# Performance work log

Measured on AMD Instinct MI355X. Metric: run time of the kernel, lower is better.

The kernel has to match this reference:

```python
import jax, jax.numpy as jnp
import numpy as np

N_WIRES = 4
BATCH, SEQ, EMBED, FFN = 8, 512, 512, 2048


def setup_inputs() -> dict:
    key = jax.random.key(0)
    k_x, k_w1, k_w2 = jax.random.split(key, 3)
    x = jax.random.normal(k_x, (BATCH, SEQ, EMBED), dtype=jnp.float32)
    # Linear params (torch Linear: y = x @ W^T + b; we store pre-transposed)
    W1 = jax.random.normal(k_w1, (EMBED, FFN), dtype=jnp.float32) / np.sqrt(EMBED)
    b1 = jnp.zeros((FFN,), dtype=jnp.float32)
    W2 = jax.random.normal(k_w2, (FFN, EMBED), dtype=jnp.float32) / np.sqrt(FFN)
    b2 = jnp.zeros((EMBED,), dtype=jnp.float32)
    return {"x": x, "W1": W1, "b1": b1, "W2": W2, "b2": b2}


def reference(x, W1, b1, W2, b2):
    b, s, d = x.shape
    flat = x.reshape(b * s, d)                      # [n, d], n = b*s
    # Quantum kernel: circuit RY(x_i) then RY(-y_i) per wire on |0..0>;
    # |0..0> amplitude = prod_i cos((x_i - y_i)/2); only first n_wires feats used
    # (reset_states(1) + states.view(-1)[0] selects batch row 0 of the reshape).
    f = flat[:, :N_WIRES]                           # [n, nw]
    half_diff = (f[:, None, :] - f[None, :, :]) * 0.5   # [n, n, nw]
    gram = jnp.abs(jnp.prod(jnp.cos(half_diff), axis=-1))  # [n, n]
    out = gram @ flat                               # [n, d]
    h = jax.nn.relu(out @ W1 + b1)                  # [n, ffn]  (dropout = eval identity)
    y = h @ W2 + b2                                 # [n, d]
    return y.reshape(b, s, d)
```

## Files before the change

### kernel.cpp

```cpp
#include <hip/hip_runtime.h>
#include <hip/hip_bf16.h>
#include <stdint.h>

using bf = __bf16;
typedef __attribute__((ext_vector_type(8))) __bf16 bf16x8;
typedef __attribute__((ext_vector_type(4))) __bf16 bf16x4;
typedef __attribute__((ext_vector_type(4))) float f32x4;
typedef __attribute__((ext_vector_type(4))) int i32x4;

#define M_TOT 4096
#define D_EMB 512
#define F_FFN 2048

__device__ __forceinline__ void gload_lds16(const void* g, void* l) {
  __builtin_amdgcn_global_load_lds(
      (const __attribute__((address_space(1))) uint32_t*)g,
      (__attribute__((address_space(3))) uint32_t*)l, 16, 0, 0);
}

__device__ __forceinline__ int swz128(int row, int b) {
  return row * 128 + (b ^ ((row & 7) << 4));
}
__device__ __forceinline__ bf16x8 ldf128(const char* base, int row, int b) {
  return *(const bf16x8*)(base + swz128(row, b));
}
__device__ __forceinline__ i32x4 ldf128i(const char* base, int row, int b) {
  return *(const i32x4*)(base + swz128(row, b));
}
template <int CHUNKS>
__device__ __forceinline__ void stage_rows4(const void* gsrc, size_t ld_bytes, char* lbase,
                                            int wave, int lane) {
  const int rsub = lane >> 3, csub = lane & 7;
  const int sc = csub ^ rsub;
#pragma unroll
  for (int i = 0; i < CHUNKS / 4; ++i) {
    int chunk = wave + i * 4;
    int row = chunk * 8 + rsub;
    gload_lds16((const char*)gsrc + (size_t)row * ld_bytes + sc * 16, lbase + chunk * 1024);
  }
}
__device__ __forceinline__ int quant_i8(float x, float s) {
  float v = x * s;
  v = fminf(127.f, fmaxf(-127.f, v));
  return (int)rintf(v);
}

#define NB_SGEN 1024
#define NT_FT   2048
#define NT_W1   1024
#define NT_W2   1024

__global__ __launch_bounds__(256) void k_prep(const float* __restrict__ x,
                                              const float* __restrict__ W1,
                                              const float* __restrict__ W2,
                                              int8_t* __restrict__ fi8, bf* __restrict__ w1T,
                                              bf* __restrict__ w2T, int8_t* __restrict__ S) {
  __shared__ __align__(16) char smem[32768];
  const int bid = blockIdx.x, tid = threadIdx.x;

  if (bid < NB_SGEN) {
    char* phiL = smem;
    char* st = smem + 16384;
    const int e = bid & 7, idx = bid >> 3;
    const int jt = e * 4 + (idx & 3);
    const int mt = idx >> 2;
    const int m0 = mt * 128;
    const int j0 = jt * 128;
    {
      int g = (tid < 128) ? (m0 + tid) : (j0 + tid - 128);
      f32x4 xv = *(const f32x4*)(x + (size_t)g * D_EMB);
      float c[4], s[4];
#pragma unroll
      for (int k = 0; k < 4; ++k) sincosf(xv[k] * 0.5f, &s[k], &c[k]);
      bf* row = (bf*)(phiL + tid * 64);
#pragma unroll
      for (int m = 0; m < 16; ++m) {
        float p = 1.0f;
#pragma unroll
        for (int k = 0; k < 4; ++k) p *= ((m >> k) & 1) ? s[k] : c[k];
        row[m] = (bf)p;
      }
#pragma unroll
      for (int m = 16; m < 32; ++m) row[m] = (bf)0.0f;
    }
    __syncthreads();

    const int wave = tid >> 6, lane = tid & 63;
    const int lr = lane & 15, lg = lane >> 4;
    const bf16x8 a0 = *(const bf16x8*)(phiL + (wave * 32 + lr) * 64 + lg * 16);
    const bf16x8 a1 = *(const bf16x8*)(phiL + (wave * 32 + 16 + lr) * 64 + lg * 16);

    const int mb0 = wave * 32 + lg * 4;
    const int key = (lr & 7) << 4;
#pragma unroll
    for (int jf = 0; jf < 8; ++jf) {
      bf16x8 b = *(const bf16x8*)(phiL + (128 + jf * 16 + lr) * 64 + lg * 16);
      f32x4 s0 = __builtin_amdgcn_mfma_f32_16x16x32_bf16(a0, b, f32x4{0.f, 0.f, 0.f, 0.f}, 0, 0, 0);
      f32x4 s1 = __builtin_amdgcn_mfma_f32_16x16x32_bf16(a1, b, f32x4{0.f, 0.f, 0.f, 0.f}, 0, 0, 0);
      uint32_t w0 = 0, w1 = 0;
#pragma unroll
      for (int r = 0; r < 4; ++r) {
        uint32_t q0 = (uint32_t)min(127, (int)rintf(fabsf(s0[r]) * 127.f));
        uint32_t q1 = (uint32_t)min(127, (int)rintf(fabsf(s1[r]) * 127.f));
        w0 |= q0 << (8 * r);
        w1 |= q1 << (8 * r);
      }
      int jrow = jf * 16 + lr;
      *(uint32_t*)(st + jrow * 128 + (mb0 ^ key)) = w0;
      *(uint32_t*)(st + jrow * 128 + ((mb0 + 16) ^ key)) = w1;
    }
    __syncthreads();
#pragma unroll
    for (int i = 0; i < 4; ++i) {
      int idx2 = tid + i * 256;
      int jrow = idx2 >> 3, seg = idx2 & 7;
      i32x4 v = *(const i32x4*)(st + jrow * 128 + ((seg * 16) ^ ((jrow & 7) << 4)));
      *(i32x4*)(S + (size_t)(j0 + jrow) * M_TOT + m0 + seg * 16) = v;
    }
    return;
  }

  float(*tile)[33] = (float(*)[33])smem;
  const int tx = tid & 31, ty = tid >> 5;
  const int cc = tid >> 3, g = tid & 7;
  if (bid < NB_SGEN + NT_FT) {
    int b2 = bid - NB_SGEN;
    int c0 = (b2 % (D_EMB / 32)) * 32, r0 = (b2 / (D_EMB / 32)) * 32;
#pragma unroll
    for (int i = 0; i < 32; i += 8)
      tile[ty + i][tx] = x[(size_t)(r0 + ty + i) * D_EMB + c0 + tx];
    __syncthreads();
    uint32_t pk = 0;
#pragma unroll
    for (int j = 0; j < 4; ++j)
      pk |= ((uint32_t)(uint8_t)(int8_t)quant_i8(tile[g * 4 + j][cc], 15.875f)) << (8 * j);
    *(uint32_t*)(fi8 + (size_t)(c0 + cc) * M_TOT + r0 + g * 4) = pk;
  } else if (bid < NB_SGEN + NT_FT + NT_W1) {
    int b2 = bid - NB_SGEN - NT_FT;
    int c0 = (b2 % (F_FFN / 32)) * 32, r0 = (b2 / (F_FFN / 32)) * 32;
#pragma unroll
    for (int i = 0; i < 32; i += 8)
      tile[ty + i][tx] = W1[(size_t)(r0 + ty + i) * F_FFN + c0 + tx];
    __syncthreads();
    bf16x4 pk;
#pragma unroll
    for (int j = 0; j < 4; ++j) pk[j] = (bf)tile[g * 4 + j][cc];
    *(bf16x4*)(w1T + (size_t)(c0 + cc) * D_EMB + r0 + g * 4) = pk;
  } else {
    int b2 = bid - NB_SGEN - NT_FT - NT_W1;
    int c0 = (b2 % (D_EMB / 32)) * 32, r0 = (b2 / (D_EMB / 32)) * 32;
#pragma unroll
    for (int i = 0; i < 32; i += 8)
      tile[ty + i][tx] = W2[(size_t)(r0 + ty + i) * D_EMB + c0 + tx];
    __syncthreads();
    bf16x4 pk;
#pragma unroll
    for (int j = 0; j < 4; ++j) pk[j] = (bf)tile[g * 4 + j][cc];
    *(bf16x4*)(w2T + (size_t)(c0 + cc) * F_FFN + r0 + g * 4) = pk;
  }
}

template <int OUTMODE>
__global__ __launch_bounds__(256, 3) void k_g64(const bf* __restrict__ A, const bf* __restrict__ BT,
                                                const float* __restrict__ bias, void* __restrict__ out,
                                                int N, int K) {
  constexpr int BUF = 16384;
  __shared__ __align__(16) char sm[3 * BUF];

  const int tid = threadIdx.x;
  const int wave = tid >> 6, lane = tid & 63;
  const int lr = lane & 15, lg = lane >> 4;
  const int wm = wave & 1, wn = wave >> 1;

  const int lin = blockIdx.x;
  const int e = lin & 7, jj = lin >> 3;
  const int bm = e * 8 + (jj & 7), bn = jj >> 3;
  const int m0 = bm * 64, n0 = bn * 64;

  f32x4 acc[2][2];
#pragma unroll
  for (int i = 0; i < 2; ++i)
#pragma unroll
    for (int f = 0; f < 2; ++f) acc[i][f] = f32x4{0.f, 0.f, 0.f, 0.f};

  const size_t ldb = (size_t)K * 2;
  stage_rows4<8>(A + (size_t)m0 * K, ldb, sm, wave, lane);
  stage_rows4<8>(BT + (size_t)n0 * K, ldb, sm + 8192, wave, lane);
  stage_rows4<8>(A + (size_t)m0 * K + 64, ldb, sm + BUF, wave, lane);
  stage_rows4<8>(BT + (size_t)n0 * K + 64, ldb, sm + BUF + 8192, wave, lane);

  const int NT = K / 64;
  for (int t = 0; t < NT; ++t) {
    char* aTc = sm + (t % 3) * BUF;
    char* bTc = aTc + 8192;
    if (t + 1 < NT) asm volatile("s_waitcnt vmcnt(4)" ::: "memory");
    else            asm volatile("s_waitcnt vmcnt(0)" ::: "memory");
    __builtin_amdgcn_s_barrier();

    if (t + 2 < NT) {
      char* aTn = sm + ((t + 2) % 3) * BUF;
      stage_rows4<8>(A + (size_t)m0 * K + (t + 2) * 64, ldb, aTn, wave, lane);
      stage_rows4<8>(BT + (size_t)n0 * K + (t + 2) * 64, ldb, aTn + 8192, wave, lane);
    }
#pragma unroll
    for (int ksl = 0; ksl < 2; ++ksl) {
      bf16x8 a[2], b[2];
#pragma unroll
      for (int i = 0; i < 2; ++i) a[i] = ldf128(aTc, wm * 32 + i * 16 + lr, (ksl * 32 + lg * 8) * 2);
#pragma unroll
      for (int f = 0; f < 2; ++f) b[f] = ldf128(bTc, wn * 32 + f * 16 + lr, (ksl * 32 + lg * 8) * 2);
#pragma unroll
      for (int i = 0; i < 2; ++i)
#pragma unroll
        for (int f = 0; f < 2; ++f)
          acc[i][f] = __builtin_amdgcn_mfma_f32_16x16x32_bf16(a[i], b[f], acc[i][f], 0, 0, 0);
    }
  }

#pragma unroll
  for (int f = 0; f < 2; ++f) {
    int n = n0 + wn * 32 + f * 16 + lr;
    float bv = bias[n];
#pragma unroll
    for (int i = 0; i < 2; ++i)
#pragma unroll
      for (int r = 0; r < 4; ++r) {
        int m = m0 + wm * 32 + i * 16 + lg * 4 + r;
        float v = acc[i][f][r] + bv;
        if (OUTMODE == 1) {
          v = v > 0.f ? v : 0.f;
          ((bf*)out)[(size_t)m * N + n] = (bf)v;
        } else {
          ((float*)out)[(size_t)m * N + n] = v;
        }
      }
  }
}

__global__ __launch_bounds__(256, 3) void k_gi64(const int8_t* __restrict__ S,
                                                 const int8_t* __restrict__ FT,
                                                 bf* __restrict__ outb) {
  constexpr int BUF = 16384;
  __shared__ __align__(16) char sm[3 * BUF];

  const int tid = threadIdx.x;
  const int wave = tid >> 6, lane = tid & 63;
  const int lr = lane & 15, lg = lane >> 4;
  const int wm = wave & 1, wn = wave >> 1;

  const int lin = blockIdx.x;
  const int e = lin & 7, jj = lin >> 3;
  const int bm = e * 8 + (jj & 7), bn = jj >> 3;
  const int m0 = bm * 64, n0 = bn * 64;

  i32x4 acc[2][2];
#pragma unroll
  for (int i = 0; i < 2; ++i)
#pragma unroll
    for (int f = 0; f < 2; ++f) acc[i][f] = i32x4{0, 0, 0, 0};

  stage_rows4<8>(S + (size_t)m0 * M_TOT, M_TOT, sm, wave, lane);
  stage_rows4<8>(FT + (size_t)n0 * M_TOT, M_TOT, sm + 8192, wave, lane);
  stage_rows4<8>(S + (size_t)m0 * M_TOT + 128, M_TOT, sm + BUF, wave, lane);
  stage_rows4<8>(FT + (size_t)n0 * M_TOT + 128, M_TOT, sm + BUF + 8192, wave, lane);

  constexpr int NT = M_TOT / 128;
  for (int t = 0; t < NT; ++t) {
    char* aTc = sm + (t % 3) * BUF;
    char* bTc = aTc + 8192;
    if (t + 1 < NT) asm volatile("s_waitcnt vmcnt(4)" ::: "memory");
    else            asm volatile("s_waitcnt vmcnt(0)" ::: "memory");
    __builtin_amdgcn_s_barrier();

    if (t + 2 < NT) {
      char* aTn = sm + ((t + 2) % 3) * BUF;
      stage_rows4<8>(S + (size_t)m0 * M_TOT + (t + 2) * 128, M_TOT, aTn, wave, lane);
      stage_rows4<8>(FT + (size_t)n0 * M_TOT + (t + 2) * 128, M_TOT, aTn + 8192, wave, lane);
    }
#pragma unroll
    for (int ksub = 0; ksub < 2; ++ksub) {
      i32x4 a[2], b[2];
#pragma unroll
      for (int i = 0; i < 2; ++i) a[i] = ldf128i(aTc, wm * 32 + i * 16 + lr, ksub * 64 + lg * 16);
#pragma unroll
      for (int f = 0; f < 2; ++f) b[f] = ldf128i(bTc, wn * 32 + f * 16 + lr, ksub * 64 + lg * 16);
#pragma unroll
      for (int i = 0; i < 2; ++i)
#pragma unroll
        for (int f = 0; f < 2; ++f)
          acc[i][f] = __builtin_amdgcn_mfma_i32_16x16x64_i8(a[i], b[f], acc[i][f], 0, 0, 0);
    }
  }

  constexpr float SCALE = 8.0f / 16129.0f;
#pragma unroll
  for (int f = 0; f < 2; ++f) {
    int n = n0 + wn * 32 + f * 16 + lr;
#pragma unroll
    for (int i = 0; i < 2; ++i)
#pragma unroll
      for (int r = 0; r < 4; ++r) {
        int m = m0 + wm * 32 + i * 16 + lg * 4 + r;
        outb[(size_t)m * D_EMB + n] = (bf)((float)acc[i][f][r] * SCALE);
      }
  }
}

constexpr size_t OFF_FI8  = 0;
constexpr size_t OFF_OUTB = OFF_FI8 + (size_t)D_EMB * M_TOT;
constexpr size_t OFF_W1T  = OFF_OUTB + (size_t)M_TOT * D_EMB * 2;
constexpr size_t OFF_W2T  = OFF_W1T + (size_t)F_FFN * D_EMB * 2;
constexpr size_t OFF_S    = OFF_W2T + (size_t)D_EMB * F_FFN * 2;
constexpr size_t OFF_HB   = OFF_S;

extern "C" void kernel_launch(void* const* d_in, const int* in_sizes, int n_in,
                              void* d_out, int out_size, void* d_ws, size_t ws_size,
                              hipStream_t stream) {
  const float* x  = (const float*)d_in[0];
  const float* W1 = (const float*)d_in[1];
  const float* b1 = (const float*)d_in[2];
  const float* W2 = (const float*)d_in[3];
  const float* b2 = (const float*)d_in[4];
  float* y = (float*)d_out;
  char* ws = (char*)d_ws;

  int8_t* fi8 = (int8_t*)(ws + OFF_FI8);
  bf* outb    = (bf*)(ws + OFF_OUTB);
  bf* w1T     = (bf*)(ws + OFF_W1T);
  bf* w2T     = (bf*)(ws + OFF_W2T);
  int8_t* S   = (int8_t*)(ws + OFF_S);
  bf* hb      = (bf*)(ws + OFF_HB);

  k_prep<<<dim3(NB_SGEN + NT_FT + NT_W1 + NT_W2), 256, 0, stream>>>(x, W1, W2, fi8, w1T, w2T, S);

  k_gi64<<<dim3(512), 256, 0, stream>>>(S, fi8, outb);

  k_g64<1><<<dim3(2048), 256, 0, stream>>>(outb, w1T, b1, (void*)hb, F_FFN, D_EMB);
  k_g64<0><<<dim3(512), 256, 0, stream>>>(hb, w2T, b2, (void*)y, D_EMB, F_FFN);
}
```

Measured before the change: 63.20 us.

## Shrink GEMM tiles to 32x64 and use double-buffered LDS for occupancy

The int8 gram GEMM and the second FFN GEMM now use 32x64 output tiles, which doubles the block count to 1024 and gives more parallelism across CUs. All GEMMs move from a triple-buffered to a double-buffered LDS pipeline with an extra barrier before the refill, and declare five blocks per CU instead of three. The aim is more resident blocks and better latency hiding, at the cost of less data reuse per tile and an extra synchronisation in every K step.

After: 70.25 us. +11.2%, slower.

```diff
diff --git a/kernel.cpp b/kernel.cpp
--- a/kernel.cpp
+++ b/kernel.cpp
@@ -32,11 +32,18 @@
                                             int wave, int lane) {
   const int rsub = lane >> 3, csub = lane & 7;
   const int sc = csub ^ rsub;
-#pragma unroll
-  for (int i = 0; i < CHUNKS / 4; ++i) {
-    int chunk = wave + i * 4;
-    int row = chunk * 8 + rsub;
-    gload_lds16((const char*)gsrc + (size_t)row * ld_bytes + sc * 16, lbase + chunk * 1024);
+  if constexpr (CHUNKS < 4) {
+    if (wave < CHUNKS) {
+      int row = wave * 8 + rsub;
+      gload_lds16((const char*)gsrc + (size_t)row * ld_bytes + sc * 16, lbase + wave * 1024);
+    }
+  } else {
+#pragma unroll
+    for (int i = 0; i < CHUNKS / 4; ++i) {
+      int chunk = wave + i * 4;
+      int row = chunk * 8 + rsub;
+      gload_lds16((const char*)gsrc + (size_t)row * ld_bytes + sc * 16, lbase + chunk * 1024);
+    }
   }
 }
 __device__ __forceinline__ int quant_i8(float x, float s) {
@@ -160,12 +167,11 @@
   }
 }
 
-template <int OUTMODE>
-__global__ __launch_bounds__(256, 3) void k_g64(const bf* __restrict__ A, const bf* __restrict__ BT,
-                                                const float* __restrict__ bias, void* __restrict__ out,
-                                                int N, int K) {
+__global__ __launch_bounds__(256, 5) void k_g64b(const bf* __restrict__ A, const bf* __restrict__ BT,
+                                                 const float* __restrict__ bias, bf* __restrict__ out,
+                                                 int N, int K) {
   constexpr int BUF = 16384;
-  __shared__ __align__(16) char sm[3 * BUF];
+  __shared__ __align__(16) char sm[2 * BUF];
 
   const int tid = threadIdx.x;
   const int wave = tid >> 6, lane = tid & 63;
@@ -191,29 +197,30 @@
 
   const int NT = K / 64;
   for (int t = 0; t < NT; ++t) {
-    char* aTc = sm + (t % 3) * BUF;
+    char* aTc = sm + (t & 1) * BUF;
     char* bTc = aTc + 8192;
     if (t + 1 < NT) asm volatile("s_waitcnt vmcnt(4)" ::: "memory");
     else            asm volatile("s_waitcnt vmcnt(0)" ::: "memory");
     __builtin_amdgcn_s_barrier();
 
+#pragma unroll
+    for (int ksl = 0; ksl < 2; ++ksl) {
+      bf16x8 a[2], b[2];
+#pragma unroll
+      for (int i = 0; i < 2; ++i) a[i] = ldf128(aTc, wm * 32 + i * 16 + lr, (ksl * 32 + lg * 8) * 2);
+#pragma unroll
+      for (int f = 0; f < 2; ++f) b[f] = ldf128(bTc, wn * 32 + f * 16 + lr, (ksl * 32 + lg * 8) * 2);
+#pragma unroll
+      for (int i = 0; i < 2; ++i)
+#pragma unroll
+        for (int f = 0; f < 2; ++f)
+          acc[i][f] = __builtin_amdgcn_mfma_f32_16x16x32_bf16(a[i], b[f], acc[i][f], 0, 0, 0);
+    }
+    __builtin_amdgcn_s_barrier();
     if (t + 2 < NT) {
-      char* aTn = sm + ((t + 2) % 3) * BUF;
+      char* aTn = sm + (t & 1) * BUF;
       stage_rows4<8>(A + (size_t)m0 * K + (t + 2) * 64, ldb, aTn, wave, lane);
       stage_rows4<8>(BT + (size_t)n0 * K + (t + 2) * 64, ldb, aTn + 8192, wave, lane);
-    }
-#pragma unroll
-    for (int ksl = 0; ksl < 2; ++ksl) {
-      bf16x8 a[2], b[2];
-#pragma unroll
-      for (int i = 0; i < 2; ++i) a[i] = ldf128(aTc, wm * 32 + i * 16 + lr, (ksl * 32 + lg * 8) * 2);
-#pragma unroll
-      for (int f = 0; f < 2; ++f) b[f] = ldf128(bTc, wn * 32 + f * 16 + lr, (ksl * 32 + lg * 8) * 2);
-#pragma unroll
-      for (int i = 0; i < 2; ++i)
-#pragma unroll
-        for (int f = 0; f < 2; ++f)
-          acc[i][f] = __builtin_amdgcn_mfma_f32_16x16x32_bf16(a[i], b[f], acc[i][f], 0, 0, 0);
     }
   }
 
@@ -227,21 +234,17 @@
       for (int r = 0; r < 4; ++r) {
         int m = m0 + wm * 32 + i * 16 + lg * 4 + r;
         float v = acc[i][f][r] + bv;
-        if (OUTMODE == 1) {
-          v = v > 0.f ? v : 0.f;
-          ((bf*)out)[(size_t)m * N + n] = (bf)v;
-        } else {
-          ((float*)out)[(size_t)m * N + n] = v;
-        }
+        v = v > 0.f ? v : 0.f;
+        out[(size_t)m * N + n] = (bf)v;
       }
   }
 }
 
-__global__ __launch_bounds__(256, 3) void k_gi64(const int8_t* __restrict__ S,
-                                                 const int8_t* __restrict__ FT,
-                                                 bf* __restrict__ outb) {
-  constexpr int BUF = 16384;
-  __shared__ __align__(16) char sm[3 * BUF];
+__global__ __launch_bounds__(256, 5) void k_g32(const bf* __restrict__ A, const bf* __restrict__ BT,
+                                                const float* __restrict__ bias, float* __restrict__ out,
+                                                int N, int K) {
+  constexpr int BUF = 12288;
+  __shared__ __align__(16) char sm[2 * BUF];
 
   const int tid = threadIdx.x;
   const int wave = tid >> 6, lane = tid & 63;
@@ -250,45 +253,101 @@
 
   const int lin = blockIdx.x;
   const int e = lin & 7, jj = lin >> 3;
-  const int bm = e * 8 + (jj & 7), bn = jj >> 3;
-  const int m0 = bm * 64, n0 = bn * 64;
-
-  i32x4 acc[2][2];
-#pragma unroll
-  for (int i = 0; i < 2; ++i)
-#pragma unroll
-    for (int f = 0; f < 2; ++f) acc[i][f] = i32x4{0, 0, 0, 0};
-
-  stage_rows4<8>(S + (size_t)m0 * M_TOT, M_TOT, sm, wave, lane);
-  stage_rows4<8>(FT + (size_t)n0 * M_TOT, M_TOT, sm + 8192, wave, lane);
-  stage_rows4<8>(S + (size_t)m0 * M_TOT + 128, M_TOT, sm + BUF, wave, lane);
-  stage_rows4<8>(FT + (size_t)n0 * M_TOT + 128, M_TOT, sm + BUF + 8192, wave, lane);
+  const int bm = e * 16 + (jj & 15), bn = jj >> 4;
+  const int m0 = bm * 32, n0 = bn * 64;
+
+  f32x4 acc[2];
+  acc[0] = f32x4{0.f, 0.f, 0.f, 0.f};
+  acc[1] = acc[0];
+
+  const size_t ldb = (size_t)K * 2;
+  stage_rows4<4>(A + (size_t)m0 * K, ldb, sm, wave, lane);
+  stage_rows4<8>(BT + (size_t)n0 * K, ldb, sm + 4096, wave, lane);
+  stage_rows4<4>(A + (size_t)m0 * K + 64, ldb, sm + BUF, wave, lane);
+  stage_rows4<8>(BT + (size_t)n0 * K + 64, ldb, sm + BUF + 4096, wave, lane);
+
+  const int NT = K / 64;
+  for (int t = 0; t < NT; ++t) {
+    char* aTc = sm + (t & 1) * BUF;
+    char* bTc = aTc + 4096;
+    if (t + 1 < NT) asm volatile("s_waitcnt vmcnt(3)" ::: "memory");
+    else            asm volatile("s_waitcnt vmcnt(0)" ::: "memory");
+    __builtin_amdgcn_s_barrier();
+
+#pragma unroll
+    for (int ksl = 0; ksl < 2; ++ksl) {
+      bf16x8 a = ldf128(aTc, wm * 16 + lr, (ksl * 32 + lg * 8) * 2);
+      bf16x8 b0 = ldf128(bTc, wn * 32 + lr, (ksl * 32 + lg * 8) * 2);
+      bf16x8 b1 = ldf128(bTc, wn * 32 + 16 + lr, (ksl * 32 + lg * 8) * 2);
+      acc[0] = __builtin_amdgcn_mfma_f32_16x16x32_bf16(a, b0, acc[0], 0, 0, 0);
+      acc[1] = __builtin_amdgcn_mfma_f32_16x16x32_bf16(a, b1, acc[1], 0, 0, 0);
+    }
+    __builtin_amdgcn_s_barrier();
+    if (t + 2 < NT) {
+      char* aTn = sm + (t & 1) * BUF;
+      stage_rows4<4>(A + (size_t)m0 * K + (t + 2) * 64, ldb, aTn, wave, lane);
+      stage_rows4<8>(BT + (size_t)n0 * K + (t + 2) * 64, ldb, aTn + 4096, wave, lane);
+    }
+  }
+
+#pragma unroll
+  for (int f = 0; f < 2; ++f) {
+    int n = n0 + wn * 32 + f * 16 + lr;
+    float bv = bias[n];
+#pragma unroll
+    for (int r = 0; r < 4; ++r) {
+      int m = m0 + wm * 16 + lg * 4 + r;
+      out[(size_t)m * N + n] = acc[f][r] + bv;
+    }
+  }
+}
+
+__global__ __launch_bounds__(256, 5) void k_gi32(const int8_t* __restrict__ S,
+                                                 const int8_t* __restrict__ FT,
+                                                 bf* __restrict__ outb) {
+  constexpr int BUF = 12288;
+  __shared__ __align__(16) char sm[2 * BUF];
+
+  const int tid = threadIdx.x;
+  const int wave = tid >> 6, lane = tid & 63;
+  const int lr = lane & 15, lg = lane >> 4;
+  const int wm = wave & 1, wn = wave >> 1;
+
+  const int lin = blockIdx.x;
+  const int e = lin & 7, jj = lin >> 3;
+  const int bm = e * 16 + (jj & 15), bn = jj >> 4;
+  const int m0 = bm * 32, n0 = bn * 64;
+
+  i32x4 acc[2];
+  acc[0] = i32x4{0, 0, 0, 0};
+  acc[1] = acc[0];
+
+  stage_rows4<4>(S + (size_t)m0 * M_TOT, M_TOT, sm, wave, lane);
+  stage_rows4<8>(FT + (size_t)n0 * M_TOT, M_TOT, sm + 4096, wave, lane);
+  stage_rows4<4>(S + (size_t)m0 * M_TOT + 128, M_TOT, sm + BUF, wave, lane);
+  stage_rows4<8>(FT + (size_t)n0 * M_TOT + 128, M_TOT, sm + BUF + 4096, wave, lane);
 
   constexpr int NT = M_TOT / 128;
   for (int t = 0; t < NT; ++t) {
-    char* aTc = sm + (t % 3) * BUF;
-    char* bTc = aTc + 8192;
-    if (t + 1 < NT) asm volatile("s_waitcnt vmcnt(4)" ::: "memory");
+    char* aTc = sm + (t & 1) * BUF;
+    char* bTc = aTc + 4096;
+    if (t + 1 < NT) asm volatile("s_waitcnt vmcnt(3)" ::: "memory");
     else            asm volatile("s_waitcnt vmcnt(0)" ::: "memory");
     __builtin_amdgcn_s_barrier();
 
+#pragma unroll
+    for (int ksub = 0; ksub < 2; ++ksub) {
+      i32x4 a = ldf128i(aTc, wm * 16 + lr, ksub * 64 + lg * 16);
+      i32x4 b0 = ldf128i(bTc, wn * 32 + lr, ksub * 64 + lg * 16);
+      i32x4 b1 = ldf128i(bTc, wn * 32 + 16 + lr, ksub * 64 + lg * 16);
+      acc[0] = __builtin_amdgcn_mfma_i32_16x16x64_i8(a, b0, acc[0], 0, 0, 0);
+      acc[1] = __builtin_amdgcn_mfma_i32_16x16x64_i8(a, b1, acc[1], 0, 0, 0);
+    }
+    __builtin_amdgcn_s_barrier();
     if (t + 2 < NT) {
-      char* aTn = sm + ((t + 2) % 3) * BUF;
-      stage_rows4<8>(S + (size_t)m0 * M_TOT + (t + 2) * 128, M_TOT, aTn, wave, lane);
-      stage_rows4<8>(FT + (size_t)n0 * M_TOT + (t + 2) * 128, M_TOT, aTn + 8192, wave, lane);
-    }
-#pragma unroll
-    for (int ksub = 0; ksub < 2; ++ksub) {
-      i32x4 a[2], b[2];
-#pragma unroll
-      for (int i = 0; i < 2; ++i) a[i] = ldf128i(aTc, wm * 32 + i * 16 + lr, ksub * 64 + lg * 16);
-#pragma unroll
-      for (int f = 0; f < 2; ++f) b[f] = ldf128i(bTc, wn * 32 + f * 16 + lr, ksub * 64 + lg * 16);
-#pragma unroll
-      for (int i = 0; i < 2; ++i)
-#pragma unroll
-        for (int f = 0; f < 2; ++f)
-          acc[i][f] = __builtin_amdgcn_mfma_i32_16x16x64_i8(a[i], b[f], acc[i][f], 0, 0, 0);
+      char* aTn = sm + (t & 1) * BUF;
+      stage_rows4<4>(S + (size_t)m0 * M_TOT + (t + 2) * 128, M_TOT, aTn, wave, lane);
+      stage_rows4<8>(FT + (size_t)n0 * M_TOT + (t + 2) * 128, M_TOT, aTn + 4096, wave, lane);
     }
   }
 
@@ -297,12 +356,10 @@
   for (int f = 0; f < 2; ++f) {
     int n = n0 + wn * 32 + f * 16 + lr;
 #pragma unroll
-    for (int i = 0; i < 2; ++i)
-#pragma unroll
-      for (int r = 0; r < 4; ++r) {
-        int m = m0 + wm * 32 + i * 16 + lg * 4 + r;
-        outb[(size_t)m * D_EMB + n] = (bf)((float)acc[i][f][r] * SCALE);
-      }
+    for (int r = 0; r < 4; ++r) {
+      int m = m0 + wm * 16 + lg * 4 + r;
+      outb[(size_t)m * D_EMB + n] = (bf)((float)acc[f][r] * SCALE);
+    }
   }
 }
 
@@ -333,8 +390,8 @@
 
   k_prep<<<dim3(NB_SGEN + NT_FT + NT_W1 + NT_W2), 256, 0, stream>>>(x, W1, W2, fi8, w1T, w2T, S);
 
-  k_gi64<<<dim3(512), 256, 0, stream>>>(S, fi8, outb);
-
-  k_g64<1><<<dim3(2048), 256, 0, stream>>>(outb, w1T, b1, (void*)hb, F_FFN, D_EMB);
-  k_g64<0><<<dim3(512), 256, 0, stream>>>(hb, w2T, b2, (void*)y, D_EMB, F_FFN);
-}
+  k_gi32<<<dim3(1024), 256, 0, stream>>>(S, fi8, outb);
+
+  k_g64b<<<dim3(2048), 256, 0, stream>>>(outb, w1T, b1, hb, F_FFN, D_EMB);
+  k_g32<<<dim3(1024), 256, 0, stream>>>(hb, w2T, b2, y, D_EMB, F_FFN);
+}
```
